# Kernel optimization log

Measured on AMD Instinct MI355X. Metric: run time of the kernel, lower is better.

## Reference

```python
import jax, jax.numpy as jnp
import numpy as np

N_NODES = 50000
N_EDGES = 800000
IN_FEATS = 96
H_FEATS = 256
N_HOPS = 3
N_NIE = N_HOPS + 1  # hops 0..3
NDIM_FC = N_NIE * H_FEATS


def setup_inputs() -> dict:
    key = jax.random.key(0)
    ks = jax.random.split(key, 8)
    edge_index = jax.random.randint(ks[0], (2, N_EDGES), 0, N_NODES, dtype=jnp.int64)
    features = jax.random.normal(ks[1], (N_NODES, IN_FEATS), dtype=jnp.float32)
    # per-hop MLP params: Linear(in_feats, h_feats) for each of n_nie hops
    s_in = 1.0 / np.sqrt(IN_FEATS)
    Ws = jax.random.uniform(ks[2], (N_NIE, IN_FEATS, H_FEATS), jnp.float32, -s_in, s_in)
    bs = jax.random.uniform(ks[3], (N_NIE, H_FEATS), jnp.float32, -s_in, s_in)
    # fusion: Linear(ndim_fc, h_feats)
    s_fc = 1.0 / np.sqrt(NDIM_FC)
    Wf = jax.random.uniform(ks[4], (NDIM_FC, H_FEATS), jnp.float32, -s_fc, s_fc)
    bf = jax.random.uniform(ks[5], (H_FEATS,), jnp.float32, -s_fc, s_fc)
    return {"edge_index": edge_index, "features": features, "Ws": Ws, "bs": bs, "Wf": Wf, "bf": bf}


def _build_norm_adj(edge_index):
    """set_diag (remove existing diag, add unit self-loops) + symmetric D^-1/2 A D^-1/2.
    Returns (rows, cols, edge_w) COO of the normalized adjacency."""
    row, col = edge_index[0].astype(jnp.int32), edge_index[1].astype(jnp.int32)
    loop = jnp.arange(N_NODES, dtype=jnp.int32)
    rows = jnp.concatenate([row, loop])
    cols = jnp.concatenate([col, loop])
    # zero out any pre-existing diagonal entries, self-loops get weight 1 (set_diag semantics)
    w = jnp.concatenate([(row != col).astype(jnp.float32), jnp.ones((N_NODES,), jnp.float32)])
    deg = jax.ops.segment_sum(w, rows, num_segments=N_NODES)
    dinv = jnp.where(deg > 0, jax.lax.rsqrt(deg), 0.0)
    edge_w = dinv[rows] * w * dinv[cols]
    return rows, cols, edge_w


def _spmm(rows, cols, edge_w, x):
    # out[r] = sum_e w_e * x[cols[e]] for edges with rows[e]==r
    return jax.ops.segment_sum(edge_w[:, None] * x[cols], rows, num_segments=N_NODES)


def reference(edge_index, features, Ws, bs, Wf, bf):
    rows, cols, edge_w = _build_norm_adj(edge_index)
    # row-normalize features (F.normalize dim=1)
    x = features / jnp.maximum(jnp.linalg.norm(features, axis=1, keepdims=True), 1e-12)
    nei_feats = [x]
    h = x
    for _ in range(N_HOPS):
        h = _spmm(rows, cols, edge_w, h)
        nei_feats.append(h)
    # per-hop MLP (dropout p=0 -> identity; norm=None -> identity) then ReLU
    ns = [jax.nn.relu(nei_feats[i] @ Ws[i] + bs[i]) for i in range(N_NIE)]
    cat = jnp.concatenate(ns, axis=1)  # [N, ndim_fc]
    out = jax.nn.relu(cat @ Wf + bf)   # [N, h_feats]
    return out
```

## Files before the change

### kernel.cpp

```cpp
#include <hip/hip_runtime.h>

#define N_NODES 50000
#define N_EDGES 800000
#define IN_F 96
#define H_F 256
#define N_NIE 4
#define SCAN_NB 196
#define BM 64
#define NBLK 782
#define LDA1 104

typedef float f32x4 __attribute__((ext_vector_type(4)));
typedef short s16x8 __attribute__((ext_vector_type(8)));
typedef unsigned short ushort;

__device__ __forceinline__ ushort bf16_rne(float f) {
    unsigned u = __float_as_uint(f);
    u += 0x7fffu + ((u >> 16) & 1u);
    return (ushort)(u >> 16);
}
__device__ __forceinline__ float bf16_f(ushort h) {
    return __uint_as_float(((unsigned)h) << 16);
}

__global__ __launch_bounds__(256) void k_count(const int* __restrict__ rows,
                                               const int* __restrict__ cols,
                                               int* __restrict__ cnt) {
    int i = blockIdx.x * 256 + threadIdx.x;
    if (i >= N_EDGES / 2) return;
    int2 r2 = ((const int2*)rows)[i];
    int2 c2 = ((const int2*)cols)[i];
    if (r2.x != c2.x) atomicAdd(&cnt[r2.x], 1);
    if (r2.y != c2.y) atomicAdd(&cnt[r2.y], 1);
}

__global__ __launch_bounds__(256) void k_scan1(const int* __restrict__ cnt,
                                               int* __restrict__ rowptr,
                                               int* __restrict__ bsum) {
    __shared__ int s[256];
    int t = threadIdx.x, e = blockIdx.x * 256 + t;
    int v = (e < N_NODES) ? cnt[e] : 0;
    s[t] = v;
    __syncthreads();
    #pragma unroll
    for (int off = 1; off < 256; off <<= 1) {
        int nv = (t >= off) ? s[t - off] : 0;
        __syncthreads();
        s[t] += nv;
        __syncthreads();
    }
    if (e < N_NODES) rowptr[e] = s[t] - v;
    if (t == 255) bsum[blockIdx.x] = s[255];
}

__global__ __launch_bounds__(256) void k_scan2(int* __restrict__ bsum,
                                               int* __restrict__ boff,
                                               int* __restrict__ rowptr) {
    __shared__ int s[256];
    int t = threadIdx.x;
    int v = (t < SCAN_NB) ? bsum[t] : 0;
    s[t] = v;
    __syncthreads();
    #pragma unroll
    for (int off = 1; off < 256; off <<= 1) {
        int nv = (t >= off) ? s[t - off] : 0;
        __syncthreads();
        s[t] += nv;
        __syncthreads();
    }
    if (t < SCAN_NB) boff[t] = s[t] - v;
    if (t == 255) rowptr[N_NODES] = s[255];
}

__global__ __launch_bounds__(256) void k_scan3(const int* __restrict__ boff,
                                               const int* __restrict__ cnt,
                                               int* __restrict__ rowptr,
                                               int* __restrict__ cursor,
                                               float* __restrict__ dinv) {
    int e = blockIdx.x * 256 + threadIdx.x;
    if (e >= N_NODES) return;
    int r = rowptr[e] + boff[blockIdx.x];
    rowptr[e] = r;
    cursor[e] = r;
    dinv[e] = rsqrtf((float)cnt[e] + 1.0f);
}

__global__ __launch_bounds__(256) void k_scatter(const int* __restrict__ rows,
                                                 const int* __restrict__ cols,
                                                 int* __restrict__ cursor,
                                                 int* __restrict__ cwi) {
    int e = blockIdx.x * 256 + threadIdx.x;
    if (e >= N_EDGES) return;
    int r = rows[e], c = cols[e];
    if (r == c) return;
    int p = atomicAdd(&cursor[r], 1);
    __builtin_nontemporal_store(c, &cwi[p]);
}

__global__ __launch_bounds__(256) void k_wsplit_ws(const float* __restrict__ src,
                                                   ushort* __restrict__ dst) {
    int idx = blockIdx.x * 256 + threadIdx.x;
    if (idx >= N_NIE * IN_F * H_F) return;
    int hop = idx / (IN_F * H_F), rem = idx % (IN_F * H_F);
    int k = rem / H_F, n = rem % H_F;
    int c = n >> 6, wc = (n >> 5) & 1, b = (n >> 4) & 1, rsel = n & 15;
    int ks = k >> 5, kk = k & 31;
    int lane = (kk >> 3) * 16 + rsel, sel8 = kk & 7;
    int d = (((((hop * 4 + c) * 2 + wc) * 2 + b) * 3 + ks) * 64 + lane) * 8 + sel8;
    dst[d] = bf16_rne(src[idx]);
}

__global__ __launch_bounds__(256) void k_wsplit_wf(const float* __restrict__ src,
                                                   ushort* __restrict__ dst) {
    int idx = blockIdx.x * 256 + threadIdx.x;
    if (idx >= N_NIE * H_F * H_F) return;
    int hop = idx / (H_F * H_F), rem = idx % (H_F * H_F);
    int k = rem / H_F, n = rem % H_F;
    int kc = k >> 5, kk = k & 31;
    int w = n >> 5, rem2 = n & 31;
    int cf = rem2 >> 4, rsel = rem2 & 15;
    int lane = (kk >> 3) * 16 + rsel, sel8 = kk & 7;
    int d = ((((hop * 8 + kc) * 8 + w) * 2 + cf) * 64 + lane) * 8 + sel8;
    dst[d] = bf16_rne(src[idx]);
}

__global__ __launch_bounds__(256) void k_norm(const float* __restrict__ feat,
                                              ushort* __restrict__ x) {
    int wid = (blockIdx.x * 256 + threadIdx.x) >> 6;
    int lane = threadIdx.x & 63;
    if (wid >= N_NODES) return;
    const float* fr = feat + (size_t)wid * IN_F;
    float v0 = (lane < IN_F) ? fr[lane] : 0.0f;
    float v1 = (lane < IN_F - 64) ? fr[64 + lane] : 0.0f;
    float ss = v0 * v0 + v1 * v1;
    #pragma unroll
    for (int o = 32; o; o >>= 1) ss += __shfl_xor(ss, o, 64);
    float inv = 1.0f / fmaxf(sqrtf(ss), 1e-12f);
    ushort* xr = x + (size_t)wid * IN_F;
    if (lane < IN_F) xr[lane] = bf16_rne(v0 * inv);
    if (lane < IN_F - 64) xr[64 + lane] = bf16_rne(v1 * inv);
}

__global__ __launch_bounds__(256) void k_spmm_csr(const int* __restrict__ rowptr,
                                                  const int* __restrict__ cwi,
                                                  const float* __restrict__ dinv,
                                                  const ushort* __restrict__ x,
                                                  ushort* __restrict__ y) {
    int g = (blockIdx.x * 256 + threadIdx.x) >> 4;
    if (g >= N_NODES) return;
    int l = threadIdx.x & 15;
    bool act = l < 12;
    float dr = dinv[g];
    s16x8 sv = {0, 0, 0, 0, 0, 0, 0, 0};
    if (act) sv = *(const s16x8*)&x[(size_t)g * IN_F + l * 8];
    float a[8] = {}, b[8] = {};
    int k = rowptr[g], e = rowptr[g + 1];
    for (; k + 3 < e; k += 4) {
        int c0 = cwi[k], c1 = cwi[k + 1], c2 = cwi[k + 2], c3 = cwi[k + 3];
        float w0 = dinv[c0], w1 = dinv[c1], w2 = dinv[c2], w3 = dinv[c3];
        s16x8 v0 = {0, 0, 0, 0, 0, 0, 0, 0}, v1 = v0, v2 = v0, v3 = v0;
        if (act) {
            v0 = *(const s16x8*)&x[(size_t)c0 * IN_F + l * 8];
            v1 = *(const s16x8*)&x[(size_t)c1 * IN_F + l * 8];
            v2 = *(const s16x8*)&x[(size_t)c2 * IN_F + l * 8];
            v3 = *(const s16x8*)&x[(size_t)c3 * IN_F + l * 8];
        }
        #pragma unroll
        for (int q = 0; q < 8; ++q) {
            a[q] += bf16_f((ushort)v0[q]) * w0 + bf16_f((ushort)v1[q]) * w1;
            b[q] += bf16_f((ushort)v2[q]) * w2 + bf16_f((ushort)v3[q]) * w3;
        }
    }
    for (; k < e; ++k) {
        int c0 = cwi[k];
        float w0 = dinv[c0];
        s16x8 v0 = {0, 0, 0, 0, 0, 0, 0, 0};
        if (act) v0 = *(const s16x8*)&x[(size_t)c0 * IN_F + l * 8];
        #pragma unroll
        for (int q = 0; q < 8; ++q) a[q] += bf16_f((ushort)v0[q]) * w0;
    }
    if (act) {
        s16x8 o;
        #pragma unroll
        for (int q = 0; q < 8; ++q)
            o[q] = (short)bf16_rne(dr * ((a[q] + b[q]) + dr * bf16_f((ushort)sv[q])));
        *(s16x8*)&y[(size_t)g * IN_F + l * 8] = o;
    }
}

__global__ __launch_bounds__(512, 4) void k_mega(const ushort* __restrict__ h0,
                                                 const ushort* __restrict__ h1,
                                                 const ushort* __restrict__ h2,
                                                 const ushort* __restrict__ h3,
                                                 const ushort* __restrict__ Ws2,
                                                 const float* __restrict__ bs,
                                                 const ushort* __restrict__ Wf2,
                                                 const float* __restrict__ bf,
                                                 float* __restrict__ out) {
    __shared__ ushort SM[23040];
    ushort* nsH = SM;
    ushort* Ah  = SM + 16384;
    float* T = (float*)SM;

    int m0 = blockIdx.x * BM;
    int tid = threadIdx.x;
    int lane = tid & 63, w = tid >> 6;
    int rsel = lane & 15, g = lane >> 4, ksel = g * 8;
    int crow = g * 4, ccol = rsel;
    int rw0 = (w & 3) * 16;
    int wc = w >> 2;
    int cwb = wc * 32;

    int sr0 = tid / 12, sj0 = tid - sr0 * 12;
    int f1 = tid + 512;
    int sr1 = f1 / 12, sj1 = f1 - sr1 * 12;
    int gm0 = m0 + sr0, gm1 = m0 + sr1;

    f32x4 acc[4][2] = {};

    {
        s16x8 v = {0, 0, 0, 0, 0, 0, 0, 0};
        if (gm0 < N_NODES) v = *(const s16x8*)&h0[(size_t)gm0 * IN_F + sj0 * 8];
        *(s16x8*)&Ah[sr0 * LDA1 + sj0 * 8] = v;
        if (tid < 256) {
            s16x8 v1 = {0, 0, 0, 0, 0, 0, 0, 0};
            if (gm1 < N_NODES) v1 = *(const s16x8*)&h0[(size_t)gm1 * IN_F + sj1 * 8];
            *(s16x8*)&Ah[sr1 * LDA1 + sj1 * 8] = v1;
        }
    }
    __syncthreads();

    for (int hop = 0; hop < N_NIE; ++hop) {
        const ushort* wsF = Ws2 + (size_t)hop * IN_F * H_F;
        const ushort* wfF = Wf2 + (size_t)hop * H_F * H_F;
        const float* bsi = bs + hop * H_F;

        #pragma unroll
        for (int c = 0; c < 4; ++c) {
            const ushort* bsrc = wsF + (size_t)((c * 2 + wc) * 2) * 3 * 64 * 8;
            f32x4 ac[2] = {};
            #pragma unroll
            for (int ks = 0; ks < 3; ++ks) {
                s16x8 ah = *(const s16x8*)&Ah[(rw0 + rsel) * LDA1 + ks * 32 + ksel];
                s16x8 b0 = *(const s16x8*)&bsrc[(size_t)(ks * 64 + lane) * 8];
                s16x8 b1 = *(const s16x8*)&bsrc[(size_t)((3 + ks) * 64 + lane) * 8];
                ac[0] = __builtin_amdgcn_mfma_f32_16x16x32_bf16(ah, b0, ac[0], 0, 0, 0);
                ac[1] = __builtin_amdgcn_mfma_f32_16x16x32_bf16(ah, b1, ac[1], 0, 0, 0);
            }
            #pragma unroll
            for (int cf = 0; cf < 2; ++cf) {
                int col = c * 64 + cwb + cf * 16 + ccol;
                float bb = bsi[col];
                #pragma unroll
                for (int ii = 0; ii < 4; ++ii) {
                    int row = rw0 + crow + ii;
                    nsH[row * 256 + (col ^ ((row & 7) << 3))] =
                        bf16_rne(fmaxf(ac[cf][ii] + bb, 0.f));
                }
            }
        }
        __syncthreads();
        if (hop < N_NIE - 1) {
            const ushort* An = (hop == 0) ? h1 : (hop == 1) ? h2 : h3;
            s16x8 pv0 = {0, 0, 0, 0, 0, 0, 0, 0}, pv1 = pv0;
            if (gm0 < N_NODES) pv0 = *(const s16x8*)&An[(size_t)gm0 * IN_F + sj0 * 8];
            if (tid < 256 && gm1 < N_NODES) pv1 = *(const s16x8*)&An[(size_t)gm1 * IN_F + sj1 * 8];
            *(s16x8*)&Ah[sr0 * LDA1 + sj0 * 8] = pv0;
            if (tid < 256) *(s16x8*)&Ah[sr1 * LDA1 + sj1 * 8] = pv1;
        }
        #pragma unroll
        for (int kc = 0; kc < 8; ++kc) {
            int k0 = kc * 32 + ksel;
            s16x8 ah4[4];
            #pragma unroll
            for (int rf = 0; rf < 4; ++rf) {
                int row = rf * 16 + rsel;
                ah4[rf] = *(const s16x8*)&nsH[row * 256 + (k0 ^ ((row & 7) << 3))];
            }
            #pragma unroll
            for (int cf = 0; cf < 2; ++cf) {
                s16x8 bh = *(const s16x8*)&wfF[(size_t)(((kc * 8 + w) * 2 + cf) * 64 + lane) * 8];
                #pragma unroll
                for (int rf = 0; rf < 4; ++rf)
                    acc[rf][cf] = __builtin_amdgcn_mfma_f32_16x16x32_bf16(ah4[rf], bh, acc[rf][cf], 0, 0, 0);
            }
        }
        __syncthreads();
    }
    #pragma unroll
    for (int half = 0; half < 2; ++half) {
        __syncthreads();
        #pragma unroll
        for (int rf2 = 0; rf2 < 2; ++rf2) {
            int rf = half * 2 + rf2;
            #pragma unroll
            for (int cf = 0; cf < 2; ++cf) {
                int col = w * 32 + cf * 16 + ccol;
                #pragma unroll
                for (int ii = 0; ii < 4; ++ii)
                    T[(rf2 * 16 + crow + ii) * 260 + col] = acc[rf][cf][ii];
            }
        }
        __syncthreads();
        #pragma unroll
        for (int p = 0; p < 4; ++p) {
            int flat = tid + p * 512;
            int r = flat >> 6, jc = flat & 63;
            int gm = m0 + half * 32 + r;
            if (gm < N_NODES) {
                f32x4 v = *(f32x4*)&T[r * 260 + jc * 4];
                f32x4 bb = *(const f32x4*)&bf[jc * 4];
                f32x4 o;
                #pragma unroll
                for (int q = 0; q < 4; ++q) o[q] = fmaxf(v[q] + bb[q], 0.f);
                *(f32x4*)&out[(size_t)gm * H_F + jc * 4] = o;
            }
        }
    }
}

extern "C" void kernel_launch(void* const* d_in, const int* in_sizes, int n_in,
                              void* d_out, int out_size, void* d_ws, size_t ws_size,
                              hipStream_t stream) {
    const int* ei = (const int*)d_in[0];
    const int* rows = ei;
    const int* cols = ei + N_EDGES;
    const float* feat = (const float*)d_in[1];
    const float* Ws = (const float*)d_in[2];
    const float* bs = (const float*)d_in[3];
    const float* Wf = (const float*)d_in[4];
    const float* bf = (const float*)d_in[5];
    float* out = (float*)d_out;

    ushort* h0 = (ushort*)d_ws;
    ushort* h1 = h0 + (size_t)N_NODES * IN_F;
    ushort* h2 = h1 + (size_t)N_NODES * IN_F;
    ushort* h3 = h2 + (size_t)N_NODES * IN_F;
    ushort* Ws2 = h3 + (size_t)N_NODES * IN_F;
    ushort* Wf2 = Ws2 + N_NIE * IN_F * H_F;
    float* dinv = (float*)(Wf2 + N_NIE * H_F * H_F);
    int* rowptr = (int*)(dinv + N_NODES);
    int* bsum = rowptr + 50004;
    int* boff = bsum + 256;
    int* cwi = boff + 256;
    int* cnt = (int*)h1;
    int* cursor = cnt + N_NODES;

    hipMemsetAsync(cnt, 0, N_NODES * sizeof(int), stream);
    k_count<<<(N_EDGES / 2 + 255) / 256, 256, 0, stream>>>(rows, cols, cnt);
    k_scan1<<<SCAN_NB, 256, 0, stream>>>(cnt, rowptr, bsum);
    k_scan2<<<1, 256, 0, stream>>>(bsum, boff, rowptr);
    k_scan3<<<SCAN_NB, 256, 0, stream>>>(boff, cnt, rowptr, cursor, dinv);
    k_scatter<<<(N_EDGES + 255) / 256, 256, 0, stream>>>(rows, cols, cursor, cwi);
    k_wsplit_ws<<<(N_NIE * IN_F * H_F + 255) / 256, 256, 0, stream>>>(Ws, Ws2);
    k_wsplit_wf<<<(N_NIE * H_F * H_F + 255) / 256, 256, 0, stream>>>(Wf, Wf2);
    k_norm<<<(N_NODES + 3) / 4, 256, 0, stream>>>(feat, h0);

    k_spmm_csr<<<(N_NODES * 16 + 255) / 256, 256, 0, stream>>>(rowptr, cwi, dinv, h0, h1);
    k_spmm_csr<<<(N_NODES * 16 + 255) / 256, 256, 0, stream>>>(rowptr, cwi, dinv, h1, h2);
    k_spmm_csr<<<(N_NODES * 16 + 255) / 256, 256, 0, stream>>>(rowptr, cwi, dinv, h2, h3);
    k_mega<<<NBLK, 512, 0, stream>>>(h0, h1, h2, h3, Ws2, bs, Wf2, bf, out);
}
```

Baseline: 302.4 us.

## Pack column index with dinv weight in CSR and merge prep kernels

The scatter kernel now stores each edge as an int2 pair holding the column index and the precomputed dinv of that column. The SpMM no longer does a dependent gather of dinv[c] for every edge in each of the three hops. Separately, the feature normalization and the two weight-reformat kernels are merged into one launch that dispatches on block index, saving two launches. In exchange the CSR edge array doubles in size, so more bytes are read per edge in each SpMM pass.

```diff
diff --git a/kernel.cpp b/kernel.cpp
--- a/kernel.cpp
+++ b/kernel.cpp
@@ -9,6 +9,9 @@
 #define BM 64
 #define NBLK 782
 #define LDA1 104
+#define PREP_NORM_NB 12500
+#define PREP_WS_NB 384
+#define PREP_WF_NB 1024
 
 typedef float f32x4 __attribute__((ext_vector_type(4)));
 typedef short s16x8 __attribute__((ext_vector_type(8)));
@@ -87,62 +90,65 @@
 
 __global__ __launch_bounds__(256) void k_scatter(const int* __restrict__ rows,
                                                  const int* __restrict__ cols,
+                                                 const float* __restrict__ dinv,
                                                  int* __restrict__ cursor,
-                                                 int* __restrict__ cwi) {
+                                                 int2* __restrict__ cw) {
     int e = blockIdx.x * 256 + threadIdx.x;
     if (e >= N_EDGES) return;
     int r = rows[e], c = cols[e];
     if (r == c) return;
     int p = atomicAdd(&cursor[r], 1);
-    __builtin_nontemporal_store(c, &cwi[p]);
-}
-
-__global__ __launch_bounds__(256) void k_wsplit_ws(const float* __restrict__ src,
-                                                   ushort* __restrict__ dst) {
-    int idx = blockIdx.x * 256 + threadIdx.x;
-    if (idx >= N_NIE * IN_F * H_F) return;
-    int hop = idx / (IN_F * H_F), rem = idx % (IN_F * H_F);
-    int k = rem / H_F, n = rem % H_F;
-    int c = n >> 6, wc = (n >> 5) & 1, b = (n >> 4) & 1, rsel = n & 15;
-    int ks = k >> 5, kk = k & 31;
-    int lane = (kk >> 3) * 16 + rsel, sel8 = kk & 7;
-    int d = (((((hop * 4 + c) * 2 + wc) * 2 + b) * 3 + ks) * 64 + lane) * 8 + sel8;
-    dst[d] = bf16_rne(src[idx]);
-}
-
-__global__ __launch_bounds__(256) void k_wsplit_wf(const float* __restrict__ src,
-                                                   ushort* __restrict__ dst) {
-    int idx = blockIdx.x * 256 + threadIdx.x;
-    if (idx >= N_NIE * H_F * H_F) return;
-    int hop = idx / (H_F * H_F), rem = idx % (H_F * H_F);
-    int k = rem / H_F, n = rem % H_F;
-    int kc = k >> 5, kk = k & 31;
-    int w = n >> 5, rem2 = n & 31;
-    int cf = rem2 >> 4, rsel = rem2 & 15;
-    int lane = (kk >> 3) * 16 + rsel, sel8 = kk & 7;
-    int d = ((((hop * 8 + kc) * 8 + w) * 2 + cf) * 64 + lane) * 8 + sel8;
-    dst[d] = bf16_rne(src[idx]);
-}
-
-__global__ __launch_bounds__(256) void k_norm(const float* __restrict__ feat,
-                                              ushort* __restrict__ x) {
-    int wid = (blockIdx.x * 256 + threadIdx.x) >> 6;
-    int lane = threadIdx.x & 63;
-    if (wid >= N_NODES) return;
-    const float* fr = feat + (size_t)wid * IN_F;
-    float v0 = (lane < IN_F) ? fr[lane] : 0.0f;
-    float v1 = (lane < IN_F - 64) ? fr[64 + lane] : 0.0f;
-    float ss = v0 * v0 + v1 * v1;
-    #pragma unroll
-    for (int o = 32; o; o >>= 1) ss += __shfl_xor(ss, o, 64);
-    float inv = 1.0f / fmaxf(sqrtf(ss), 1e-12f);
-    ushort* xr = x + (size_t)wid * IN_F;
-    if (lane < IN_F) xr[lane] = bf16_rne(v0 * inv);
-    if (lane < IN_F - 64) xr[64 + lane] = bf16_rne(v1 * inv);
+    long long v = ((long long)(unsigned)__float_as_int(dinv[c]) << 32) | (unsigned)c;
+    __builtin_nontemporal_store(v, (long long*)&cw[p]);
+}
+
+__global__ __launch_bounds__(256) void k_prep(const float* __restrict__ feat,
+                                              ushort* __restrict__ x,
+                                              const float* __restrict__ Ws,
+                                              ushort* __restrict__ Ws2,
+                                              const float* __restrict__ Wf,
+                                              ushort* __restrict__ Wf2) {
+    int blk = blockIdx.x;
+    if (blk < PREP_NORM_NB) {
+        int wid = (blk * 256 + threadIdx.x) >> 6;
+        int lane = threadIdx.x & 63;
+        if (wid >= N_NODES) return;
+        const float* fr = feat + (size_t)wid * IN_F;
+        float v0 = (lane < IN_F) ? fr[lane] : 0.0f;
+        float v1 = (lane < IN_F - 64) ? fr[64 + lane] : 0.0f;
+        float ss = v0 * v0 + v1 * v1;
+        #pragma unroll
+        for (int o = 32; o; o >>= 1) ss += __shfl_xor(ss, o, 64);
+        float inv = 1.0f / fmaxf(sqrtf(ss), 1e-12f);
+        ushort* xr = x + (size_t)wid * IN_F;
+        if (lane < IN_F) xr[lane] = bf16_rne(v0 * inv);
+        if (lane < IN_F - 64) xr[64 + lane] = bf16_rne(v1 * inv);
+    } else if (blk < PREP_NORM_NB + PREP_WS_NB) {
+        int idx = (blk - PREP_NORM_NB) * 256 + threadIdx.x;
+        if (idx >= N_NIE * IN_F * H_F) return;
+        int hop = idx / (IN_F * H_F), rem = idx % (IN_F * H_F);
+        int k = rem / H_F, n = rem % H_F;
+        int c = n >> 6, wc = (n >> 5) & 1, b = (n >> 4) & 1, rsel = n & 15;
+        int ks = k >> 5, kk = k & 31;
+        int lane = (kk >> 3) * 16 + rsel, sel8 = kk & 7;
+        int d = (((((hop * 4 + c) * 2 + wc) * 2 + b) * 3 + ks) * 64 + lane) * 8 + sel8;
+        Ws2[d] = bf16_rne(Ws[idx]);
+    } else {
+        int idx = (blk - PREP_NORM_NB - PREP_WS_NB) * 256 + threadIdx.x;
+        if (idx >= N_NIE * H_F * H_F) return;
+        int hop = idx / (H_F * H_F), rem = idx % (H_F * H_F);
+        int k = rem / H_F, n = rem % H_F;
+        int kc = k >> 5, kk = k & 31;
+        int w = n >> 5, rem2 = n & 31;
+        int cf = rem2 >> 4, rsel = rem2 & 15;
+        int lane = (kk >> 3) * 16 + rsel, sel8 = kk & 7;
+        int d = ((((hop * 8 + kc) * 8 + w) * 2 + cf) * 64 + lane) * 8 + sel8;
+        Wf2[d] = bf16_rne(Wf[idx]);
+    }
 }
 
 __global__ __launch_bounds__(256) void k_spmm_csr(const int* __restrict__ rowptr,
-                                                  const int* __restrict__ cwi,
+                                                  const int2* __restrict__ cw,
                                                   const float* __restrict__ dinv,
                                                   const ushort* __restrict__ x,
                                                   ushort* __restrict__ y) {
@@ -156,14 +162,15 @@
     float a[8] = {}, b[8] = {};
     int k = rowptr[g], e = rowptr[g + 1];
     for (; k + 3 < e; k += 4) {
-        int c0 = cwi[k], c1 = cwi[k + 1], c2 = cwi[k + 2], c3 = cwi[k + 3];
-        float w0 = dinv[c0], w1 = dinv[c1], w2 = dinv[c2], w3 = dinv[c3];
+        int2 p0 = cw[k], p1 = cw[k + 1], p2 = cw[k + 2], p3 = cw[k + 3];
+        float w0 = __int_as_float(p0.y), w1 = __int_as_float(p1.y);
+        float w2 = __int_as_float(p2.y), w3 = __int_as_float(p3.y);
         s16x8 v0 = {0, 0, 0, 0, 0, 0, 0, 0}, v1 = v0, v2 = v0, v3 = v0;
         if (act) {
-            v0 = *(const s16x8*)&x[(size_t)c0 * IN_F + l * 8];
-            v1 = *(const s16x8*)&x[(size_t)c1 * IN_F + l * 8];
-            v2 = *(const s16x8*)&x[(size_t)c2 * IN_F + l * 8];
-            v3 = *(const s16x8*)&x[(size_t)c3 * IN_F + l * 8];
+            v0 = *(const s16x8*)&x[(size_t)p0.x * IN_F + l * 8];
+            v1 = *(const s16x8*)&x[(size_t)p1.x * IN_F + l * 8];
+            v2 = *(const s16x8*)&x[(size_t)p2.x * IN_F + l * 8];
+            v3 = *(const s16x8*)&x[(size_t)p3.x * IN_F + l * 8];
         }
         #pragma unroll
         for (int q = 0; q < 8; ++q) {
@@ -172,10 +179,10 @@
         }
     }
     for (; k < e; ++k) {
-        int c0 = cwi[k];
-        float w0 = dinv[c0];
+        int2 p0 = cw[k];
+        float w0 = __int_as_float(p0.y);
         s16x8 v0 = {0, 0, 0, 0, 0, 0, 0, 0};
-        if (act) v0 = *(const s16x8*)&x[(size_t)c0 * IN_F + l * 8];
+        if (act) v0 = *(const s16x8*)&x[(size_t)p0.x * IN_F + l * 8];
         #pragma unroll
         for (int q = 0; q < 8; ++q) a[q] += bf16_f((ushort)v0[q]) * w0;
     }
@@ -342,7 +349,7 @@
     int* rowptr = (int*)(dinv + N_NODES);
     int* bsum = rowptr + 50004;
     int* boff = bsum + 256;
-    int* cwi = boff + 256;
+    int2* cw = (int2*)(boff + 256);
     int* cnt = (int*)h1;
     int* cursor = cnt + N_NODES;
 
@@ -351,13 +358,12 @@
     k_scan1<<<SCAN_NB, 256, 0, stream>>>(cnt, rowptr, bsum);
     k_scan2<<<1, 256, 0, stream>>>(bsum, boff, rowptr);
     k_scan3<<<SCAN_NB, 256, 0, stream>>>(boff, cnt, rowptr, cursor, dinv);
-    k_scatter<<<(N_EDGES + 255) / 256, 256, 0, stream>>>(rows, cols, cursor, cwi);
-    k_wsplit_ws<<<(N_NIE * IN_F * H_F + 255) / 256, 256, 0, stream>>>(Ws, Ws2);
-    k_wsplit_wf<<<(N_NIE * H_F * H_F + 255) / 256, 256, 0, stream>>>(Wf, Wf2);
-    k_norm<<<(N_NODES + 3) / 4, 256, 0, stream>>>(feat, h0);
-
-    k_spmm_csr<<<(N_NODES * 16 + 255) / 256, 256, 0, stream>>>(rowptr, cwi, dinv, h0, h1);
-    k_spmm_csr<<<(N_NODES * 16 + 255) / 256, 256, 0, stream>>>(rowptr, cwi, dinv, h1, h2);
-    k_spmm_csr<<<(N_NODES * 16 + 255) / 256, 256, 0, stream>>>(rowptr, cwi, dinv, h2, h3);
+    k_scatter<<<(N_EDGES + 255) / 256, 256, 0, stream>>>(rows, cols, dinv, cursor, cw);
+    k_prep<<<PREP_NORM_NB + PREP_WS_NB + PREP_WF_NB, 256, 0, stream>>>(feat, h0, Ws, Ws2,
+                                                                       Wf, Wf2);
+
+    k_spmm_csr<<<(N_NODES * 16 + 255) / 256, 256, 0, stream>>>(rowptr, cw, dinv, h0, h1);
+    k_spmm_csr<<<(N_NODES * 16 + 255) / 256, 256, 0, stream>>>(rowptr, cw, dinv, h1, h2);
+    k_spmm_csr<<<(N_NODES * 16 + 255) / 256, 256, 0, stream>>>(rowptr, cw, dinv, h2, h3);
     k_mega<<<NBLK, 512, 0, stream>>>(h0, h1, h2, h3, Ws2, bs, Wf2, bf, out);
 }
```

Result: faster. 295.8 us (-2.2%).
